# Optimization experiments

Hardware: AMD Instinct MI355X
Metric: run time of the kernel (lower is better)

The kernel has to match this reference:

```python
import jax, jax.numpy as jnp
import numpy as np

N = 50000      # nodes
D = 128        # in_dim
O = 128        # out_dim
MAX_DEG = 32   # degrees uniform in [0, MAX_DEG]


def setup_inputs() -> dict:
    rng = np.random.default_rng(0)
    deg = rng.integers(0, MAX_DEG + 1, size=N)          # includes deg==0 nodes
    dst = np.repeat(np.arange(N), deg)                  # target node per edge (grouped, like the buckets)
    E = dst.shape[0]                                    # ~800000
    src = rng.integers(0, N, size=E)                    # neighbor index per edge (flat neighbor_list)

    key = jax.random.key(0)
    k1, k2, k3, k4 = jax.random.split(key, 4)
    scale = jnp.float32(1.0 / np.sqrt(D))
    return {
        "x":  jax.random.normal(k1, (N, D), jnp.float32),
        "Wg": jax.random.normal(k2, (O, D), jnp.float32) * scale,  # global_lin.weight
        "Wl": jax.random.normal(k3, (O, D), jnp.float32) * scale,  # local_lin.weight
        "Ws": jax.random.normal(k4, (O, D), jnp.float32) * scale,  # self_lin.weight
        "b":  jnp.zeros((O,), jnp.float32),                        # bias param
        "src": jnp.asarray(src, jnp.int32),
        "dst": jnp.asarray(dst, jnp.int32),
        "deg": jnp.asarray(deg, jnp.int32),
    }


def reference(x, Wg, Wl, Ws, b, src, dst, deg):
    n = x.shape[0]
    # global branch: applied to every node
    g_out = x @ Wg.T                                           # [N, O]
    # mean-aggregate neighbor features (gather + segment-sum == the per-bucket view().mean())
    neigh_sum = jax.ops.segment_sum(x[src], dst, num_segments=n)   # [N, D]
    degf = jnp.maximum(deg, 1).astype(x.dtype)[:, None]
    neigh_mean = neigh_sum * (1.0 / degf)                       # [N, D]
    # local + self branches only for deg > 0 (deg==0 bucket keeps just global_out)
    mask = (deg > 0).astype(x.dtype)[:, None]                   # [N, 1]
    out = g_out + mask * (neigh_mean @ Wl.T + x @ Ws.T) + b
    # dropout is identity in eval mode; ELU activation
    return jax.nn.elu(out)
```

## Files before the change

### kernel.cpp

```cpp
#include <hip/hip_runtime.h>
#include <cstdint>
#include <cstddef>

#define GNPB 8
#define MNPB 16
#define GAST 264
#define DFRNG 512
#define VP_BLOCKS 16
#define VPG_BLOCKS 8

typedef __attribute__((ext_vector_type(8))) short bf16x8;
typedef __attribute__((ext_vector_type(4))) float f32x4;

static __device__ __forceinline__ unsigned short f2bf(float f) {
    unsigned int u = __builtin_bit_cast(unsigned int, f);
    u += 0x7fffu + ((u >> 16) & 1u);
    return (unsigned short)(u >> 16);
}
static __device__ __forceinline__ float bfhi(unsigned int u) { return __builtin_bit_cast(float, u & 0xFFFF0000u); }
static __device__ __forceinline__ float bflo(unsigned int u) { return __builtin_bit_cast(float, u << 16); }
static __device__ __forceinline__ void acc8(float* a, const uint4& v, unsigned m) {
    unsigned x0 = v.x & m, x1 = v.y & m, x2 = v.z & m, x3 = v.w & m;
    a[0] += bflo(x0); a[1] += bfhi(x0); a[2] += bflo(x1); a[3] += bfhi(x1);
    a[4] += bflo(x2); a[5] += bfhi(x2); a[6] += bflo(x3); a[7] += bfhi(x3);
}

__global__ __launch_bounds__(256)
void prep(const float* __restrict__ x, const float* __restrict__ Wg,
          const float* __restrict__ Wl, const float* __restrict__ Ws,
          const int* __restrict__ dst,
          unsigned short* __restrict__ Vp, unsigned short* __restrict__ Vpg,
          unsigned short* __restrict__ xb, int* __restrict__ blkoff,
          int total8, int nblk_g, int noffb, int E) {
    const int bx = blockIdx.x, t = threadIdx.x;
    if (bx < VP_BLOCKS) {
        int gid = bx * 256 + t;
        if (gid < 4096) {
            int l = gid & 63, srow = (gid >> 6) & 7, g = gid >> 9;
            int o = g * 16 + (l & 15);
            int k = srow * 32 + (l >> 4) * 8;
            uint4 u;
            if (k < 128) {
                const float* pg = Wg + o * 128 + k;
                const float* ps = Ws + o * 128 + k;
                u.x = (unsigned)f2bf(pg[0]+ps[0]) | ((unsigned)f2bf(pg[1]+ps[1]) << 16);
                u.y = (unsigned)f2bf(pg[2]+ps[2]) | ((unsigned)f2bf(pg[3]+ps[3]) << 16);
                u.z = (unsigned)f2bf(pg[4]+ps[4]) | ((unsigned)f2bf(pg[5]+ps[5]) << 16);
                u.w = (unsigned)f2bf(pg[6]+ps[6]) | ((unsigned)f2bf(pg[7]+ps[7]) << 16);
            } else {
                const float* pl = Wl + o * 128 + (k - 128);
                u.x = (unsigned)f2bf(pl[0]) | ((unsigned)f2bf(pl[1]) << 16);
                u.y = (unsigned)f2bf(pl[2]) | ((unsigned)f2bf(pl[3]) << 16);
                u.z = (unsigned)f2bf(pl[4]) | ((unsigned)f2bf(pl[5]) << 16);
                u.w = (unsigned)f2bf(pl[6]) | ((unsigned)f2bf(pl[7]) << 16);
            }
            ((uint4*)Vp)[gid] = u;
        }
    } else if (bx < VP_BLOCKS + VPG_BLOCKS) {
        int gid = (bx - VP_BLOCKS) * 256 + t;
        if (gid < 2048) {
            int l = gid & 63, s = (gid >> 6) & 3, g = gid >> 8;
            int o = g * 16 + (l & 15);
            int k = s * 32 + (l >> 4) * 8;
            const float* p = Wg + o * 128 + k;
            uint4 u;
            u.x = (unsigned)f2bf(p[0]) | ((unsigned)f2bf(p[1]) << 16);
            u.y = (unsigned)f2bf(p[2]) | ((unsigned)f2bf(p[3]) << 16);
            u.z = (unsigned)f2bf(p[4]) | ((unsigned)f2bf(p[5]) << 16);
            u.w = (unsigned)f2bf(p[6]) | ((unsigned)f2bf(p[7]) << 16);
            ((uint4*)Vpg)[gid] = u;
        }
    } else if (bx < VP_BLOCKS + VPG_BLOCKS + noffb) {
        int b = (bx - VP_BLOCKS - VPG_BLOCKS) * 256 + t;
        if (b < nblk_g) {
            int target = b * GNPB;
            int lo = 0, hi = E;
            while (lo < hi) { int mid = (lo + hi) >> 1; if (dst[mid] < target) lo = mid + 1; else hi = mid; }
            blkoff[b] = lo;
        }
    } else {
        int gid = (bx - VP_BLOCKS - VPG_BLOCKS - noffb) * 256 + t;
        if (gid < total8) {
            const float4* px = (const float4*)x + (size_t)gid * 2;
            float4 a = px[0], bq = px[1];
            uint4 u;
            u.x = (unsigned)f2bf(a.x)  | ((unsigned)f2bf(a.y)  << 16);
            u.y = (unsigned)f2bf(a.z)  | ((unsigned)f2bf(a.w)  << 16);
            u.z = (unsigned)f2bf(bq.x) | ((unsigned)f2bf(bq.y) << 16);
            u.w = (unsigned)f2bf(bq.z) | ((unsigned)f2bf(bq.w) << 16);
            ((uint4*)xb)[gid] = u;
        }
    }
}

__global__ __launch_bounds__(512, 5)
void ggemm(const unsigned short* __restrict__ xb, const int* __restrict__ src,
           const int* __restrict__ deg, const int* __restrict__ blkoff,
           const unsigned short* __restrict__ Vp, const unsigned short* __restrict__ Vpg,
           const float* __restrict__ bias, float* __restrict__ out, int N, int ngemm) {
    __shared__ __align__(16) unsigned short As[MNPB * GAST];
    const int t = threadIdx.x, wv = t >> 6, lane = t & 63;
    const int c = lane & 15, p = lane >> 4;

    if (blockIdx.x >= ngemm) {
        __shared__ int nds[DFRNG];
        __shared__ int ncnt;
        const int rb = (blockIdx.x - ngemm) * DFRNG;
        if (t == 0) ncnt = 0;
        __syncthreads();
        {
            int n = rb + t;
            if (n < N && deg[n] == 0) nds[atomicAdd(&ncnt, 1)] = n;
        }
        __syncthreads();
        const int cnt = ncnt;
        if (cnt == 0) return;
        const bf16x8* VB = (const bf16x8*)Vpg;
        const int col = wv * 16 + c;
        const float bv = bias[col];
        for (int base = 0; base < cnt; base += 16) {
            if (t < 256) {
                int row = t >> 4, ch = t & 15;
                int i = base + row; if (i > cnt - 1) i = cnt - 1;
                int node = nds[i];
                *(uint4*)(As + row * GAST + ch * 8) =
                    *(const uint4*)(xb + (size_t)node * 128 + ch * 8);
            }
            bf16x8 b0 = VB[(wv * 4) * 64 + lane];
            __syncthreads();
            f32x4 acc = (f32x4){0.f, 0.f, 0.f, 0.f};
#pragma unroll
            for (int s2 = 0; s2 < 4; ++s2) {
                int sn = (s2 + 1) & 3;
                bf16x8 n0 = VB[(wv * 4 + sn) * 64 + lane];
                bf16x8 a0 = *(const bf16x8*)(As + c * GAST + s2 * 32 + p * 8);
                acc = __builtin_amdgcn_mfma_f32_16x16x32_bf16(a0, b0, acc, 0, 0, 0);
                b0 = n0;
            }
#pragma unroll
            for (int reg = 0; reg < 4; ++reg) {
                int i = base + p * 4 + reg;
                if (i < cnt) {
                    int n = nds[i];
                    float v = acc[reg] + bv;
                    out[(size_t)n * 128 + col] = (v > 0.f) ? v : __expf(v) - 1.0f;
                }
            }
            __syncthreads();
        }
        return;
    }

    const int base = blockIdx.x * MNPB;
    if (t < 256) {
        int row = t >> 4, ch = t & 15;
        int grow = base + row; if (grow > N - 1) grow = N - 1;
        *(uint4*)(As + row * GAST + ch * 8) =
            *(const uint4*)(xb + (size_t)grow * 128 + ch * 8);
    }

    int dg16 = 0;
    if (lane < 16 && base + lane < N) dg16 = deg[base + lane];
    int incl = dg16;
#pragma unroll
    for (int off = 1; off < 16; off <<= 1) {
        int v = __shfl_up(incl, off, 64);
        if (lane >= off) incl += v;
    }
    const int blk_s = blkoff[blockIdx.x * 2];
    const uint4* x4 = (const uint4*)xb;

#pragma unroll 1
    for (int half = 0; half < 2; ++half) {
        const int j = wv + half * 8;
        const int d = __shfl(dg16, j, 64);
        const int s = blk_s + __shfl(incl, j, 64) - d;
        const bool valid = (base + j < N);

        int idx = 0;
        if (valid && lane < d) idx = src[s + lane];

        int r0 = __shfl(idx, p, 64),      r1 = __shfl(idx, p + 4, 64);
        int r2 = __shfl(idx, p + 8, 64),  r3 = __shfl(idx, p + 12, 64);
        uint4 v0 = x4[(size_t)r0 * 16 + c], v1 = x4[(size_t)r1 * 16 + c];
        uint4 v2 = x4[(size_t)r2 * 16 + c], v3 = x4[(size_t)r3 * 16 + c];
        uint4 v4, v5, v6, v7;
        const bool two = (d > 16);
        if (two) {
            int e = 16 + p;
            int r4 = __shfl(idx, e, 64),      r5 = __shfl(idx, e + 4, 64);
            int r6 = __shfl(idx, e + 8, 64),  r7 = __shfl(idx, e + 12, 64);
            v4 = x4[(size_t)r4 * 16 + c]; v5 = x4[(size_t)r5 * 16 + c];
            v6 = x4[(size_t)r6 * 16 + c]; v7 = x4[(size_t)r7 * 16 + c];
        }
        float a[8] = {0,0,0,0,0,0,0,0};
        float b[8] = {0,0,0,0,0,0,0,0};
        acc8(a, v0, (p      < d) ? ~0u : 0u);
        acc8(b, v1, (p + 4  < d) ? ~0u : 0u);
        acc8(a, v2, (p + 8  < d) ? ~0u : 0u);
        acc8(b, v3, (p + 12 < d) ? ~0u : 0u);
        if (two) {
            int e = 16 + p;
            acc8(a, v4, (e      < d) ? ~0u : 0u);
            acc8(b, v5, (e + 4  < d) ? ~0u : 0u);
            acc8(a, v6, (e + 8  < d) ? ~0u : 0u);
            acc8(b, v7, (e + 12 < d) ? ~0u : 0u);
        }
#pragma unroll
        for (int i = 0; i < 8; ++i) a[i] += b[i];
#pragma unroll
        for (int i = 0; i < 8; ++i) {
            a[i] += __shfl_xor(a[i], 16, 64);
            a[i] += __shfl_xor(a[i], 32, 64);
        }
        if (p == 0 && valid) {
            float inv = (d > 0) ? 1.0f / (float)d : 0.0f;
            uint4 u;
            u.x = (unsigned)f2bf(a[0]*inv) | ((unsigned)f2bf(a[1]*inv) << 16);
            u.y = (unsigned)f2bf(a[2]*inv) | ((unsigned)f2bf(a[3]*inv) << 16);
            u.z = (unsigned)f2bf(a[4]*inv) | ((unsigned)f2bf(a[5]*inv) << 16);
            u.w = (unsigned)f2bf(a[6]*inv) | ((unsigned)f2bf(a[7]*inv) << 16);
            *(uint4*)(As + j * GAST + 128 + c * 8) = u;
        }
    }

    const bf16x8* VB = (const bf16x8*)Vp;
    bf16x8 b0 = VB[(wv * 8) * 64 + lane];
    __syncthreads();

    f32x4 acc = (f32x4){0.f, 0.f, 0.f, 0.f};
#pragma unroll
    for (int s2 = 0; s2 < 8; ++s2) {
        int sn = (s2 + 1) & 7;
        bf16x8 n0 = VB[(wv * 8 + sn) * 64 + lane];
        bf16x8 a0 = *(const bf16x8*)(As + c * GAST + s2 * 32 + p * 8);
        acc = __builtin_amdgcn_mfma_f32_16x16x32_bf16(a0, b0, acc, 0, 0, 0);
        b0 = n0;
    }

    const int col = wv * 16 + c;
    const float bv = bias[col];
#pragma unroll
    for (int reg = 0; reg < 4; ++reg) {
        int lrow = p * 4 + reg;
        int grow = base + lrow;
        int rdeg = __shfl(dg16, lrow, 64);
        if (grow < N && rdeg > 0) {
            float v = acc[reg] + bv;
            out[(size_t)grow * 128 + col] = (v > 0.f) ? v : __expf(v) - 1.0f;
        }
    }
}

extern "C" void kernel_launch(void* const* d_in, const int* in_sizes, int n_in,
                              void* d_out, int out_size, void* d_ws, size_t ws_size,
                              hipStream_t stream) {
    const float* x  = (const float*)d_in[0];
    const float* Wg = (const float*)d_in[1];
    const float* Wl = (const float*)d_in[2];
    const float* Ws = (const float*)d_in[3];
    const float* b  = (const float*)d_in[4];
    const int*   src = (const int*)d_in[5];
    const int*   dst = (const int*)d_in[6];
    const int*   deg = (const int*)d_in[7];
    const int E = in_sizes[5];
    const int N = in_sizes[7];
    float* out = (float*)d_out;

    unsigned short* Vp     = (unsigned short*)d_ws;
    unsigned short* Vpg    = (unsigned short*)((char*)d_ws + 65536);
    int*            blkoff = (int*)((char*)d_ws + 98304);
    unsigned short* xb     = (unsigned short*)((char*)d_ws + 131072);

    const int nblk_g = (N + GNPB - 1) / GNPB;
    const int noffb  = (nblk_g + 255) / 256;
    const int total8 = N * 16;
    const int nconv  = (total8 + 255) / 256;
    const int ngemm  = (N + MNPB - 1) / MNPB;
    const int ndeg   = (N + DFRNG - 1) / DFRNG;

    prep<<<dim3(VP_BLOCKS + VPG_BLOCKS + noffb + nconv), dim3(256), 0, stream>>>(
        x, Wg, Wl, Ws, dst, Vp, Vpg, xb, blkoff, total8, nblk_g, noffb, E);
    ggemm<<<dim3(ngemm + ndeg), dim3(512), 0, stream>>>(
        xb, src, deg, blkoff, Vp, Vpg, b, out, N, ngemm);
}
```

Measured before the change: 139.7 us.

## Issue both nodes' neighbor gathers together using a zero sentinel row

The two sequential per-wave node iterations are unrolled so the gather loads for both nodes are issued before any accumulation, which raises memory-level parallelism. A zero row is appended to the bf16 copy of x, and invalid neighbor slots point at it, so the per-element masking in the accumulation is dropped. The zero-degree blocks are moved to the front of the grid, and the occupancy hint drops from 5 to 4 waves per SIMD to make room for the extra live registers. The cost is higher register pressure and an extra padded row in the workspace.

```diff
diff --git a/kernel.cpp b/kernel.cpp
--- a/kernel.cpp
+++ b/kernel.cpp
@@ -19,10 +19,9 @@
 }
 static __device__ __forceinline__ float bfhi(unsigned int u) { return __builtin_bit_cast(float, u & 0xFFFF0000u); }
 static __device__ __forceinline__ float bflo(unsigned int u) { return __builtin_bit_cast(float, u << 16); }
-static __device__ __forceinline__ void acc8(float* a, const uint4& v, unsigned m) {
-    unsigned x0 = v.x & m, x1 = v.y & m, x2 = v.z & m, x3 = v.w & m;
-    a[0] += bflo(x0); a[1] += bfhi(x0); a[2] += bflo(x1); a[3] += bfhi(x1);
-    a[4] += bflo(x2); a[5] += bfhi(x2); a[6] += bflo(x3); a[7] += bfhi(x3);
+static __device__ __forceinline__ void add8(float* a, const uint4& v) {
+    a[0] += bflo(v.x); a[1] += bfhi(v.x); a[2] += bflo(v.y); a[3] += bfhi(v.y);
+    a[4] += bflo(v.z); a[5] += bfhi(v.z); a[6] += bflo(v.w); a[7] += bfhi(v.w);
 }
 
 __global__ __launch_bounds__(256)
@@ -89,23 +88,25 @@
             u.z = (unsigned)f2bf(bq.x) | ((unsigned)f2bf(bq.y) << 16);
             u.w = (unsigned)f2bf(bq.z) | ((unsigned)f2bf(bq.w) << 16);
             ((uint4*)xb)[gid] = u;
-        }
-    }
-}
-
-__global__ __launch_bounds__(512, 5)
+        } else if (gid < total8 + 16) {
+            ((uint4*)xb)[gid] = (uint4){0u, 0u, 0u, 0u};
+        }
+    }
+}
+
+__global__ __launch_bounds__(512, 4)
 void ggemm(const unsigned short* __restrict__ xb, const int* __restrict__ src,
            const int* __restrict__ deg, const int* __restrict__ blkoff,
            const unsigned short* __restrict__ Vp, const unsigned short* __restrict__ Vpg,
-           const float* __restrict__ bias, float* __restrict__ out, int N, int ngemm) {
+           const float* __restrict__ bias, float* __restrict__ out, int N, int ndeg) {
     __shared__ __align__(16) unsigned short As[MNPB * GAST];
     const int t = threadIdx.x, wv = t >> 6, lane = t & 63;
     const int c = lane & 15, p = lane >> 4;
 
-    if (blockIdx.x >= ngemm) {
+    if (blockIdx.x < ndeg) {
         __shared__ int nds[DFRNG];
         __shared__ int ncnt;
-        const int rb = (blockIdx.x - ngemm) * DFRNG;
+        const int rb = blockIdx.x * DFRNG;
         if (t == 0) ncnt = 0;
         __syncthreads();
         {
@@ -151,7 +152,8 @@
         return;
     }
 
-    const int base = blockIdx.x * MNPB;
+    const int bid = blockIdx.x - ndeg;
+    const int base = bid * MNPB;
     if (t < 256) {
         int row = t >> 4, ch = t & 15;
         int grow = base + row; if (grow > N - 1) grow = N - 1;
@@ -167,45 +169,51 @@
         int v = __shfl_up(incl, off, 64);
         if (lane >= off) incl += v;
     }
-    const int blk_s = blkoff[blockIdx.x * 2];
+    const int blk_s = blkoff[bid * 2];
     const uint4* x4 = (const uint4*)xb;
 
-#pragma unroll 1
-    for (int half = 0; half < 2; ++half) {
-        const int j = wv + half * 8;
-        const int d = __shfl(dg16, j, 64);
-        const int s = blk_s + __shfl(incl, j, 64) - d;
-        const bool valid = (base + j < N);
-
-        int idx = 0;
-        if (valid && lane < d) idx = src[s + lane];
-
-        int r0 = __shfl(idx, p, 64),      r1 = __shfl(idx, p + 4, 64);
-        int r2 = __shfl(idx, p + 8, 64),  r3 = __shfl(idx, p + 12, 64);
-        uint4 v0 = x4[(size_t)r0 * 16 + c], v1 = x4[(size_t)r1 * 16 + c];
-        uint4 v2 = x4[(size_t)r2 * 16 + c], v3 = x4[(size_t)r3 * 16 + c];
-        uint4 v4, v5, v6, v7;
-        const bool two = (d > 16);
-        if (two) {
-            int e = 16 + p;
-            int r4 = __shfl(idx, e, 64),      r5 = __shfl(idx, e + 4, 64);
-            int r6 = __shfl(idx, e + 8, 64),  r7 = __shfl(idx, e + 12, 64);
-            v4 = x4[(size_t)r4 * 16 + c]; v5 = x4[(size_t)r5 * 16 + c];
-            v6 = x4[(size_t)r6 * 16 + c]; v7 = x4[(size_t)r7 * 16 + c];
-        }
+    const int jA = wv, jB = wv + 8;
+    const int dA = __shfl(dg16, jA, 64), dB = __shfl(dg16, jB, 64);
+    const int sA = blk_s + __shfl(incl, jA, 64) - dA;
+    const int sB = blk_s + __shfl(incl, jB, 64) - dB;
+    const bool vA = (base + jA < N), vB = (base + jB < N);
+
+    int idxA = N, idxB = N;
+    if (vA && lane < dA) idxA = src[sA + lane];
+    if (vB && lane < dB) idxB = src[sB + lane];
+
+    int a0i = __shfl(idxA, p, 64),      a1i = __shfl(idxA, p + 4, 64);
+    int a2i = __shfl(idxA, p + 8, 64),  a3i = __shfl(idxA, p + 12, 64);
+    uint4 vA0 = x4[(size_t)a0i * 16 + c], vA1 = x4[(size_t)a1i * 16 + c];
+    uint4 vA2 = x4[(size_t)a2i * 16 + c], vA3 = x4[(size_t)a3i * 16 + c];
+    uint4 vA4, vA5, vA6, vA7;
+    const bool twoA = (dA > 16);
+    if (twoA) {
+        int e = 16 + p;
+        int a4i = __shfl(idxA, e, 64),      a5i = __shfl(idxA, e + 4, 64);
+        int a6i = __shfl(idxA, e + 8, 64),  a7i = __shfl(idxA, e + 12, 64);
+        vA4 = x4[(size_t)a4i * 16 + c]; vA5 = x4[(size_t)a5i * 16 + c];
+        vA6 = x4[(size_t)a6i * 16 + c]; vA7 = x4[(size_t)a7i * 16 + c];
+    }
+    int b0i = __shfl(idxB, p, 64),      b1i = __shfl(idxB, p + 4, 64);
+    int b2i = __shfl(idxB, p + 8, 64),  b3i = __shfl(idxB, p + 12, 64);
+    uint4 vB0 = x4[(size_t)b0i * 16 + c], vB1 = x4[(size_t)b1i * 16 + c];
+    uint4 vB2 = x4[(size_t)b2i * 16 + c], vB3 = x4[(size_t)b3i * 16 + c];
+    uint4 vB4, vB5, vB6, vB7;
+    const bool twoB = (dB > 16);
+    if (twoB) {
+        int e = 16 + p;
+        int b4i = __shfl(idxB, e, 64),      b5i = __shfl(idxB, e + 4, 64);
+        int b6i = __shfl(idxB, e + 8, 64),  b7i = __shfl(idxB, e + 12, 64);
+        vB4 = x4[(size_t)b4i * 16 + c]; vB5 = x4[(size_t)b5i * 16 + c];
+        vB6 = x4[(size_t)b6i * 16 + c]; vB7 = x4[(size_t)b7i * 16 + c];
+    }
+
+    {
         float a[8] = {0,0,0,0,0,0,0,0};
         float b[8] = {0,0,0,0,0,0,0,0};
-        acc8(a, v0, (p      < d) ? ~0u : 0u);
-        acc8(b, v1, (p + 4  < d) ? ~0u : 0u);
-        acc8(a, v2, (p + 8  < d) ? ~0u : 0u);
-        acc8(b, v3, (p + 12 < d) ? ~0u : 0u);
-        if (two) {
-            int e = 16 + p;
-            acc8(a, v4, (e      < d) ? ~0u : 0u);
-            acc8(b, v5, (e + 4  < d) ? ~0u : 0u);
-            acc8(a, v6, (e + 8  < d) ? ~0u : 0u);
-            acc8(b, v7, (e + 12 < d) ? ~0u : 0u);
-        }
+        add8(a, vA0); add8(b, vA1); add8(a, vA2); add8(b, vA3);
+        if (twoA) { add8(a, vA4); add8(b, vA5); add8(a, vA6); add8(b, vA7); }
 #pragma unroll
         for (int i = 0; i < 8; ++i) a[i] += b[i];
 #pragma unroll
@@ -213,14 +221,36 @@
             a[i] += __shfl_xor(a[i], 16, 64);
             a[i] += __shfl_xor(a[i], 32, 64);
         }
-        if (p == 0 && valid) {
-            float inv = (d > 0) ? 1.0f / (float)d : 0.0f;
+        if (p == 0 && vA) {
+            float inv = (dA > 0) ? 1.0f / (float)dA : 0.0f;
             uint4 u;
             u.x = (unsigned)f2bf(a[0]*inv) | ((unsigned)f2bf(a[1]*inv) << 16);
             u.y = (unsigned)f2bf(a[2]*inv) | ((unsigned)f2bf(a[3]*inv) << 16);
             u.z = (unsigned)f2bf(a[4]*inv) | ((unsigned)f2bf(a[5]*inv) << 16);
             u.w = (unsigned)f2bf(a[6]*inv) | ((unsigned)f2bf(a[7]*inv) << 16);
-            *(uint4*)(As + j * GAST + 128 + c * 8) = u;
+            *(uint4*)(As + jA * GAST + 128 + c * 8) = u;
+        }
+    }
+    {
+        float a[8] = {0,0,0,0,0,0,0,0};
+        float b[8] = {0,0,0,0,0,0,0,0};
+        add8(a, vB0); add8(b, vB1); add8(a, vB2); add8(b, vB3);
+        if (twoB) { add8(a, vB4); add8(b, vB5); add8(a, vB6); add8(b, vB7); }
+#pragma unroll
+        for (int i = 0; i < 8; ++i) a[i] += b[i];
+#pragma unroll
+        for (int i = 0; i < 8; ++i) {
+            a[i] += __shfl_xor(a[i], 16, 64);
+            a[i] += __shfl_xor(a[i], 32, 64);
+        }
+        if (p == 0 && vB) {
+            float inv = (dB > 0) ? 1.0f / (float)dB : 0.0f;
+            uint4 u;
+            u.x = (unsigned)f2bf(a[0]*inv) | ((unsigned)f2bf(a[1]*inv) << 16);
+            u.y = (unsigned)f2bf(a[2]*inv) | ((unsigned)f2bf(a[3]*inv) << 16);
+            u.z = (unsigned)f2bf(a[4]*inv) | ((unsigned)f2bf(a[5]*inv) << 16);
+            u.w = (unsigned)f2bf(a[6]*inv) | ((unsigned)f2bf(a[7]*inv) << 16);
+            *(uint4*)(As + jB * GAST + 128 + c * 8) = u;
         }
     }
 
@@ -275,12 +305,12 @@
     const int nblk_g = (N + GNPB - 1) / GNPB;
     const int noffb  = (nblk_g + 255) / 256;
     const int total8 = N * 16;
-    const int nconv  = (total8 + 255) / 256;
+    const int nconv  = (total8 + 16 + 255) / 256;
     const int ngemm  = (N + MNPB - 1) / MNPB;
     const int ndeg   = (N + DFRNG - 1) / DFRNG;
 
     prep<<<dim3(VP_BLOCKS + VPG_BLOCKS + noffb + nconv), dim3(256), 0, stream>>>(
         x, Wg, Wl, Ws, dst, Vp, Vpg, xb, blkoff, total8, nblk_g, noffb, E);
     ggemm<<<dim3(ngemm + ndeg), dim3(512), 0, stream>>>(
-        xb, src, deg, blkoff, Vp, Vpg, b, out, N, ngemm);
-}
+        xb, src, deg, blkoff, Vp, Vpg, b, out, N, ndeg);
+}
```

After: 136.1 us. 1.03x faster.

## Process eight nodes per block with one gather pass and a zero padding row

Applied to the files above, without the earlier changes.

The fused gather+GEMM kernel now handles 8 nodes per 512-thread block, one node per wave, instead of 16 nodes in two serial halves. A zeroed padding row is appended to the bf16 copy of x, and invalid neighbor slots point to it, so the per-slot mask work is dropped. The zero-degree blocks move to the front of the grid and the occupancy hint drops from 5 to 4. This doubles the block count and halves the MFMA row usage, since only 8 of 16 rows are real. The aim is more memory-level parallelism in the random gather, traded for extra block and GEMM overhead.

```diff
diff --git a/kernel.cpp b/kernel.cpp
--- a/kernel.cpp
+++ b/kernel.cpp
@@ -2,8 +2,7 @@
 #include <cstdint>
 #include <cstddef>
 
-#define GNPB 8
-#define MNPB 16
+#define NPB 8
 #define GAST 264
 #define DFRNG 512
 #define VP_BLOCKS 16
@@ -19,10 +18,9 @@
 }
 static __device__ __forceinline__ float bfhi(unsigned int u) { return __builtin_bit_cast(float, u & 0xFFFF0000u); }
 static __device__ __forceinline__ float bflo(unsigned int u) { return __builtin_bit_cast(float, u << 16); }
-static __device__ __forceinline__ void acc8(float* a, const uint4& v, unsigned m) {
-    unsigned x0 = v.x & m, x1 = v.y & m, x2 = v.z & m, x3 = v.w & m;
-    a[0] += bflo(x0); a[1] += bfhi(x0); a[2] += bflo(x1); a[3] += bfhi(x1);
-    a[4] += bflo(x2); a[5] += bfhi(x2); a[6] += bflo(x3); a[7] += bfhi(x3);
+static __device__ __forceinline__ void add8(float* a, const uint4& v) {
+    a[0] += bflo(v.x); a[1] += bfhi(v.x); a[2] += bflo(v.y); a[3] += bfhi(v.y);
+    a[4] += bflo(v.z); a[5] += bfhi(v.z); a[6] += bflo(v.w); a[7] += bfhi(v.w);
 }
 
 __global__ __launch_bounds__(256)
@@ -73,7 +71,7 @@
     } else if (bx < VP_BLOCKS + VPG_BLOCKS + noffb) {
         int b = (bx - VP_BLOCKS - VPG_BLOCKS) * 256 + t;
         if (b < nblk_g) {
-            int target = b * GNPB;
+            int target = b * NPB;
             int lo = 0, hi = E;
             while (lo < hi) { int mid = (lo + hi) >> 1; if (dst[mid] < target) lo = mid + 1; else hi = mid; }
             blkoff[b] = lo;
@@ -89,23 +87,25 @@
             u.z = (unsigned)f2bf(bq.x) | ((unsigned)f2bf(bq.y) << 16);
             u.w = (unsigned)f2bf(bq.z) | ((unsigned)f2bf(bq.w) << 16);
             ((uint4*)xb)[gid] = u;
-        }
-    }
-}
-
-__global__ __launch_bounds__(512, 5)
+        } else if (gid < total8 + 16) {
+            ((uint4*)xb)[gid] = (uint4){0u, 0u, 0u, 0u};
+        }
+    }
+}
+
+__global__ __launch_bounds__(512, 4)
 void ggemm(const unsigned short* __restrict__ xb, const int* __restrict__ src,
            const int* __restrict__ deg, const int* __restrict__ blkoff,
            const unsigned short* __restrict__ Vp, const unsigned short* __restrict__ Vpg,
-           const float* __restrict__ bias, float* __restrict__ out, int N, int ngemm) {
-    __shared__ __align__(16) unsigned short As[MNPB * GAST];
+           const float* __restrict__ bias, float* __restrict__ out, int N, int ndeg) {
+    __shared__ __align__(16) unsigned short As[16 * GAST];
     const int t = threadIdx.x, wv = t >> 6, lane = t & 63;
     const int c = lane & 15, p = lane >> 4;
 
-    if (blockIdx.x >= ngemm) {
+    if (blockIdx.x < ndeg) {
         __shared__ int nds[DFRNG];
         __shared__ int ncnt;
-        const int rb = (blockIdx.x - ngemm) * DFRNG;
+        const int rb = blockIdx.x * DFRNG;
         if (t == 0) ncnt = 0;
         __syncthreads();
         {
@@ -151,77 +151,64 @@
         return;
     }
 
-    const int base = blockIdx.x * MNPB;
-    if (t < 256) {
+    const int bid = blockIdx.x - ndeg;
+    const int base = bid * NPB;
+    if (t < 128) {
         int row = t >> 4, ch = t & 15;
         int grow = base + row; if (grow > N - 1) grow = N - 1;
         *(uint4*)(As + row * GAST + ch * 8) =
             *(const uint4*)(xb + (size_t)grow * 128 + ch * 8);
     }
 
-    int dg16 = 0;
-    if (lane < 16 && base + lane < N) dg16 = deg[base + lane];
-    int incl = dg16;
-#pragma unroll
-    for (int off = 1; off < 16; off <<= 1) {
+    int dg8 = 0;
+    if (lane < NPB && base + lane < N) dg8 = deg[base + lane];
+    int incl = dg8;
+#pragma unroll
+    for (int off = 1; off < NPB; off <<= 1) {
         int v = __shfl_up(incl, off, 64);
         if (lane >= off) incl += v;
     }
-    const int blk_s = blkoff[blockIdx.x * 2];
+    const int d = __shfl(dg8, wv, 64);
+    const int s = blkoff[bid] + __shfl(incl, wv, 64) - d;
+    const int n = base + wv;
+    const bool vN = (n < N);
+
+    int idx = N;
+    if (vN && lane < d) idx = src[s + lane];
+
     const uint4* x4 = (const uint4*)xb;
-
-#pragma unroll 1
-    for (int half = 0; half < 2; ++half) {
-        const int j = wv + half * 8;
-        const int d = __shfl(dg16, j, 64);
-        const int s = blk_s + __shfl(incl, j, 64) - d;
-        const bool valid = (base + j < N);
-
-        int idx = 0;
-        if (valid && lane < d) idx = src[s + lane];
-
-        int r0 = __shfl(idx, p, 64),      r1 = __shfl(idx, p + 4, 64);
-        int r2 = __shfl(idx, p + 8, 64),  r3 = __shfl(idx, p + 12, 64);
-        uint4 v0 = x4[(size_t)r0 * 16 + c], v1 = x4[(size_t)r1 * 16 + c];
-        uint4 v2 = x4[(size_t)r2 * 16 + c], v3 = x4[(size_t)r3 * 16 + c];
-        uint4 v4, v5, v6, v7;
-        const bool two = (d > 16);
-        if (two) {
-            int e = 16 + p;
-            int r4 = __shfl(idx, e, 64),      r5 = __shfl(idx, e + 4, 64);
-            int r6 = __shfl(idx, e + 8, 64),  r7 = __shfl(idx, e + 12, 64);
-            v4 = x4[(size_t)r4 * 16 + c]; v5 = x4[(size_t)r5 * 16 + c];
-            v6 = x4[(size_t)r6 * 16 + c]; v7 = x4[(size_t)r7 * 16 + c];
-        }
-        float a[8] = {0,0,0,0,0,0,0,0};
-        float b[8] = {0,0,0,0,0,0,0,0};
-        acc8(a, v0, (p      < d) ? ~0u : 0u);
-        acc8(b, v1, (p + 4  < d) ? ~0u : 0u);
-        acc8(a, v2, (p + 8  < d) ? ~0u : 0u);
-        acc8(b, v3, (p + 12 < d) ? ~0u : 0u);
-        if (two) {
-            int e = 16 + p;
-            acc8(a, v4, (e      < d) ? ~0u : 0u);
-            acc8(b, v5, (e + 4  < d) ? ~0u : 0u);
-            acc8(a, v6, (e + 8  < d) ? ~0u : 0u);
-            acc8(b, v7, (e + 12 < d) ? ~0u : 0u);
-        }
-#pragma unroll
-        for (int i = 0; i < 8; ++i) a[i] += b[i];
-#pragma unroll
-        for (int i = 0; i < 8; ++i) {
-            a[i] += __shfl_xor(a[i], 16, 64);
-            a[i] += __shfl_xor(a[i], 32, 64);
-        }
-        if (p == 0 && valid) {
-            float inv = (d > 0) ? 1.0f / (float)d : 0.0f;
-            uint4 u;
-            u.x = (unsigned)f2bf(a[0]*inv) | ((unsigned)f2bf(a[1]*inv) << 16);
-            u.y = (unsigned)f2bf(a[2]*inv) | ((unsigned)f2bf(a[3]*inv) << 16);
-            u.z = (unsigned)f2bf(a[4]*inv) | ((unsigned)f2bf(a[5]*inv) << 16);
-            u.w = (unsigned)f2bf(a[6]*inv) | ((unsigned)f2bf(a[7]*inv) << 16);
-            *(uint4*)(As + j * GAST + 128 + c * 8) = u;
-        }
+    int r0 = __shfl(idx, p, 64),      r1 = __shfl(idx, p + 4, 64);
+    int r2 = __shfl(idx, p + 8, 64),  r3 = __shfl(idx, p + 12, 64);
+    uint4 v0 = x4[(size_t)r0 * 16 + c], v1 = x4[(size_t)r1 * 16 + c];
+    uint4 v2 = x4[(size_t)r2 * 16 + c], v3 = x4[(size_t)r3 * 16 + c];
+    float a[8] = {0,0,0,0,0,0,0,0};
+    float b[8] = {0,0,0,0,0,0,0,0};
+    if (d > 16) {
+        int e = 16 + p;
+        int r4 = __shfl(idx, e, 64),      r5 = __shfl(idx, e + 4, 64);
+        int r6 = __shfl(idx, e + 8, 64),  r7 = __shfl(idx, e + 12, 64);
+        uint4 v4 = x4[(size_t)r4 * 16 + c], v5 = x4[(size_t)r5 * 16 + c];
+        uint4 v6 = x4[(size_t)r6 * 16 + c], v7 = x4[(size_t)r7 * 16 + c];
+        add8(a, v0); add8(b, v1); add8(a, v2); add8(b, v3);
+        add8(a, v4); add8(b, v5); add8(a, v6); add8(b, v7);
+    } else {
+        add8(a, v0); add8(b, v1); add8(a, v2); add8(b, v3);
+    }
+#pragma unroll
+    for (int i = 0; i < 8; ++i) a[i] += b[i];
+#pragma unroll
+    for (int i = 0; i < 8; ++i) {
+        a[i] += __shfl_xor(a[i], 16, 64);
+        a[i] += __shfl_xor(a[i], 32, 64);
+    }
+    if (p == 0 && vN) {
+        float inv = (d > 0) ? 1.0f / (float)d : 0.0f;
+        uint4 u;
+        u.x = (unsigned)f2bf(a[0]*inv) | ((unsigned)f2bf(a[1]*inv) << 16);
+        u.y = (unsigned)f2bf(a[2]*inv) | ((unsigned)f2bf(a[3]*inv) << 16);
+        u.z = (unsigned)f2bf(a[4]*inv) | ((unsigned)f2bf(a[5]*inv) << 16);
+        u.w = (unsigned)f2bf(a[6]*inv) | ((unsigned)f2bf(a[7]*inv) << 16);
+        *(uint4*)(As + wv * GAST + 128 + c * 8) = u;
     }
 
     const bf16x8* VB = (const bf16x8*)Vp;
@@ -243,11 +230,13 @@
 #pragma unroll
     for (int reg = 0; reg < 4; ++reg) {
         int lrow = p * 4 + reg;
-        int grow = base + lrow;
-        int rdeg = __shfl(dg16, lrow, 64);
-        if (grow < N && rdeg > 0) {
-            float v = acc[reg] + bv;
-            out[(size_t)grow * 128 + col] = (v > 0.f) ? v : __expf(v) - 1.0f;
+        if (lrow < NPB) {
+            int grow = base + lrow;
+            int rdeg = __shfl(dg8, lrow & 7, 64);
+            if (grow < N && rdeg > 0) {
+                float v = acc[reg] + bv;
+                out[(size_t)grow * 128 + col] = (v > 0.f) ? v : __expf(v) - 1.0f;
+            }
         }
     }
 }
@@ -272,15 +261,14 @@
     int*            blkoff = (int*)((char*)d_ws + 98304);
     unsigned short* xb     = (unsigned short*)((char*)d_ws + 131072);
 
-    const int nblk_g = (N + GNPB - 1) / GNPB;
+    const int nblk_g = (N + NPB - 1) / NPB;
     const int noffb  = (nblk_g + 255) / 256;
     const int total8 = N * 16;
-    const int nconv  = (total8 + 255) / 256;
-    const int ngemm  = (N + MNPB - 1) / MNPB;
+    const int nconv  = (total8 + 16 + 255) / 256;
     const int ndeg   = (N + DFRNG - 1) / DFRNG;
 
     prep<<<dim3(VP_BLOCKS + VPG_BLOCKS + noffb + nconv), dim3(256), 0, stream>>>(
         x, Wg, Wl, Ws, dst, Vp, Vpg, xb, blkoff, total8, nblk_g, noffb, E);
-    ggemm<<<dim3(ngemm + ndeg), dim3(512), 0, stream>>>(
-        xb, src, deg, blkoff, Vp, Vpg, b, out, N, ngemm);
-}
+    ggemm<<<dim3(nblk_g + ndeg), dim3(512), 0, stream>>>(
+        xb, src, deg, blkoff, Vp, Vpg, b, out, N, ndeg);
+}
```

Result: no change. 141.9 us (+1.6%).
